# Kernel optimization log

Hardware: AMD Instinct MI355X
Metric: run time of the kernel (lower is better)

## Reference

```python
import jax, jax.numpy as jnp
import numpy as np


def setup_inputs() -> dict:
    key = jax.random.key(0)
    k1, k2 = jax.random.split(key)
    B, Ld, Lq, D = 32, 2048, 512, 256
    doc = jax.random.normal(k1, (B, Ld, D), dtype=jnp.float32)
    query = jax.random.normal(k2, (B, Lq, D), dtype=jnp.float32)
    doc_mask = jnp.ones((B, Ld), dtype=jnp.float32)
    q_mask = jnp.ones((B, Lq), dtype=jnp.float32)
    return {"doc": doc, "query": query, "doc_mask": doc_mask, "q_mask": q_mask}


def reference(doc, query, doc_mask, q_mask):
    # match_score: [B, Lq, Ld] = tanh(query @ doc^T)
    match_score = jnp.tanh(jnp.einsum('bqd,btd->bqt', query, doc))
    # sum over query positions -> [B, Ld]; softmax over doc positions
    query_to_doc_att = jax.nn.softmax(jnp.sum(match_score, axis=1), axis=-1)
    # sum over doc positions -> [B, Lq]; softmax over query positions
    doc_to_query_att = jax.nn.softmax(jnp.sum(match_score, axis=-1), axis=-1)
    # mask and renormalize
    alpha = query_to_doc_att * doc_mask
    alpha = alpha / jnp.sum(alpha, axis=1, keepdims=True)
    beta = doc_to_query_att * q_mask
    beta = beta / jnp.sum(beta, axis=1, keepdims=True)
    # weighted pooling: doc^T @ alpha -> [B, D]; query^T @ beta -> [B, D]
    doc_vector = jnp.einsum('btd,bt->bd', doc, alpha)
    que_vector = jnp.einsum('bqd,bq->bd', query, beta)
    return jnp.concatenate([doc_vector, que_vector], axis=1)  # [B, 2D]
```

## Files before the change

### kernel.cpp

```cpp
#include <hip/hip_runtime.h>
#include <hip/hip_bf16.h>
#include <cstdint>

#define BB 32
#define LD 2048
#define LQ 512
#define DD 256
#define BM 128
#define BN 128
#define BK 64

typedef _Float16 half8 __attribute__((ext_vector_type(8)));
typedef _Float16 half4 __attribute__((ext_vector_type(4)));
typedef float float4v __attribute__((ext_vector_type(4)));

__device__ __forceinline__ float tanh_fast(float x) {
    float e = __expf(2.0f * x);
    return 1.0f - 2.0f / (e + 1.0f);
}

__device__ __forceinline__ void load_lds16(const void* g, void* s) {
    __builtin_amdgcn_global_load_lds((const __attribute__((address_space(1))) void*)g,
                                     (__attribute__((address_space(3))) void*)s, 16, 0, 0);
}

#define DOCN8 (BB * LD * DD / 8)
#define QRYN8 (BB * LQ * DD / 8)

__global__ __launch_bounds__(256) void kconv(const float* __restrict__ doc,
                                             const float* __restrict__ qry,
                                             _Float16* __restrict__ dh,
                                             _Float16* __restrict__ qh) {
    int i = blockIdx.x * 256 + threadIdx.x;
    const float* src;
    _Float16* dst;
    int idx;
    if (i < DOCN8) { src = doc; dst = dh; idx = i; }
    else           { src = qry; dst = qh; idx = i - DOCN8; }
    const float4v* s = (const float4v*)src + (size_t)idx * 2;
    float4v a = s[0], c = s[1];
    half8 h = {(_Float16)a[0], (_Float16)a[1], (_Float16)a[2], (_Float16)a[3],
               (_Float16)c[0], (_Float16)c[1], (_Float16)c[2], (_Float16)c[3]};
    *((half8*)dst + idx) = h;
}

template <bool F16SRC>
__global__ __launch_bounds__(256) void k1(const void* __restrict__ qsrc,
                                          const void* __restrict__ dsrc,
                                          float* __restrict__ alog,
                                          float* __restrict__ blog) {
    __shared__ _Float16 sQ[BM * BK];
    __shared__ _Float16 sD[BN * BK];
    const int bq = blockIdx.x, bt = blockIdx.y, b = blockIdx.z;
    const int tid = threadIdx.x;
    const int lane = tid & 63;
    const int wave = tid >> 6;
    const int r16 = lane & 15;
    const int q4 = lane >> 4;
    const int mb = (wave >> 1) * 64, nb = (wave & 1) * 64;

    float4v acc[4][4];
    float4v zero = {0.f, 0.f, 0.f, 0.f};
#pragma unroll
    for (int m = 0; m < 4; m++)
#pragma unroll
        for (int n = 0; n < 4; n++) acc[m][n] = zero;

    const int lrow = lane >> 3;
    const int lcol = ((lane & 7) ^ lrow) * 8;

    for (int kk = 0; kk < DD; kk += BK) {
        __syncthreads();
        if constexpr (F16SRC) {
            const _Float16* Qh = (const _Float16*)qsrc + ((size_t)b * LQ + bq * BM) * DD;
            const _Float16* Dh = (const _Float16*)dsrc + ((size_t)b * LD + bt * BN) * DD;
#pragma unroll
            for (int j = 0; j < 4; j++) {
                int c = wave * 4 + j;
                int row = 8 * c + lrow;
                load_lds16(Qh + (size_t)row * DD + kk + lcol, &sQ[c * 512]);
                load_lds16(Dh + (size_t)row * DD + kk + lcol, &sD[c * 512]);
            }
        } else {
            const float* Qf = (const float*)qsrc + ((size_t)b * LQ + bq * BM) * DD;
            const float* Df = (const float*)dsrc + ((size_t)b * LD + bt * BN) * DD;
#pragma unroll
            for (int i = 0; i < 8; i++) {
                int f = tid + 256 * i;
                int row = f >> 4, c = f & 15;
                int c2 = c >> 1, hlf = c & 1;
                int p = c2 ^ (row & 7);
                float4v v = *(const float4v*)(Qf + (size_t)row * DD + kk + 4 * c);
                half4 h = {(_Float16)v[0], (_Float16)v[1], (_Float16)v[2], (_Float16)v[3]};
                *(half4*)(&sQ[row * BK + p * 8 + hlf * 4]) = h;
                float4v w = *(const float4v*)(Df + (size_t)row * DD + kk + 4 * c);
                half4 h2 = {(_Float16)w[0], (_Float16)w[1], (_Float16)w[2], (_Float16)w[3]};
                *(half4*)(&sD[row * BK + p * 8 + hlf * 4]) = h2;
            }
        }
        __syncthreads();

#pragma unroll
        for (int kk2 = 0; kk2 < 2; kk2++) {
            const int sw = ((4 * kk2 + q4) ^ (r16 & 7)) * 8;
            half8 af[4], bf[4];
#pragma unroll
            for (int m = 0; m < 4; m++) af[m] = *(const half8*)(&sQ[(mb + 16 * m + r16) * BK + sw]);
#pragma unroll
            for (int n = 0; n < 4; n++) bf[n] = *(const half8*)(&sD[(nb + 16 * n + r16) * BK + sw]);
#pragma unroll
            for (int m = 0; m < 4; m++)
#pragma unroll
                for (int n = 0; n < 4; n++)
                    acc[m][n] = __builtin_amdgcn_mfma_f32_16x16x32_f16(af[m], bf[n], acc[m][n], 0, 0, 0);
        }
    }

    float rsum[4][4];
    float csum[4];
#pragma unroll
    for (int m = 0; m < 4; m++)
#pragma unroll
        for (int r = 0; r < 4; r++) rsum[m][r] = 0.f;
#pragma unroll
    for (int n = 0; n < 4; n++) csum[n] = 0.f;

#pragma unroll
    for (int m = 0; m < 4; m++)
#pragma unroll
        for (int n = 0; n < 4; n++) {
            float t0 = tanh_fast(acc[m][n][0]);
            float t1 = tanh_fast(acc[m][n][1]);
            float t2 = tanh_fast(acc[m][n][2]);
            float t3 = tanh_fast(acc[m][n][3]);
            csum[n] += t0 + t1 + t2 + t3;
            rsum[m][0] += t0;
            rsum[m][1] += t1;
            rsum[m][2] += t2;
            rsum[m][3] += t3;
        }

#pragma unroll
    for (int m = 0; m < 4; m++) {
#pragma unroll
        for (int r = 0; r < 4; r++) {
            float v = rsum[m][r];
            v += __shfl_xor(v, 1);
            v += __shfl_xor(v, 2);
            v += __shfl_xor(v, 4);
            v += __shfl_xor(v, 8);
            rsum[m][r] = v;
        }
        if (r16 < 4) {
            float v = (r16 == 0) ? rsum[m][0] : (r16 == 1) ? rsum[m][1] : (r16 == 2) ? rsum[m][2] : rsum[m][3];
            atomicAdd(blog + b * LQ + bq * BM + mb + 16 * m + 4 * q4 + r16, v);
        }
    }
#pragma unroll
    for (int n = 0; n < 4; n++) {
        float v = csum[n];
        v += __shfl_xor(v, 16);
        v += __shfl_xor(v, 32);
        if (lane < 16) atomicAdd(alog + b * LD + bt * BN + nb + 16 * n + lane, v);
    }
}

__global__ __launch_bounds__(256) void k2(const float* __restrict__ alog, const float* __restrict__ blog,
                                          const float* __restrict__ dmask, const float* __restrict__ qmask,
                                          float* __restrict__ alpha, float* __restrict__ beta) {
    int blk = blockIdx.x;
    const float *lg, *mk;
    float* out;
    int n;
    if (blk < BB) {
        lg = alog + blk * LD; mk = dmask + blk * LD; out = alpha + blk * LD; n = LD;
    } else {
        int b = blk - BB;
        lg = blog + b * LQ; mk = qmask + b * LQ; out = beta + b * LQ; n = LQ;
    }
    int tid = threadIdx.x, lane = tid & 63, wave = tid >> 6;
    __shared__ float sm[4], ss[4];
    float mx = -3.0e38f;
    for (int i = tid; i < n; i += 256) mx = fmaxf(mx, lg[i]);
#pragma unroll
    for (int s = 1; s < 64; s <<= 1) mx = fmaxf(mx, __shfl_xor(mx, s));
    if (lane == 0) sm[wave] = mx;
    __syncthreads();
    mx = fmaxf(fmaxf(sm[0], sm[1]), fmaxf(sm[2], sm[3]));
    float sum = 0.f;
    for (int i = tid; i < n; i += 256) sum += __expf(lg[i] - mx) * mk[i];
#pragma unroll
    for (int s = 1; s < 64; s <<= 1) sum += __shfl_xor(sum, s);
    if (lane == 0) ss[wave] = sum;
    __syncthreads();
    sum = ss[0] + ss[1] + ss[2] + ss[3];
    float inv = 1.0f / sum;
    for (int i = tid; i < n; i += 256) out[i] = __expf(lg[i] - mx) * mk[i] * inv;
}

template <bool F16SRC>
__global__ __launch_bounds__(256) void k3(const float* __restrict__ docf, const float* __restrict__ qryf,
                                          const _Float16* __restrict__ dh, const _Float16* __restrict__ qh,
                                          const float* __restrict__ alpha, const float* __restrict__ beta,
                                          float* __restrict__ out) {
    __shared__ float sm[8 * DD];
    int blk = blockIdx.x, tid = threadIdx.x;
    const _Float16* srch;
    const float* srcf;
    const float* w;
    float* dst;
    if (blk < BB * 16) {
        int b = blk >> 4, ch = blk & 15;
        srch = dh + ((size_t)b * LD + ch * 128) * DD;
        srcf = docf + ((size_t)b * LD + ch * 128) * DD;
        w = alpha + b * LD + ch * 128;
        dst = out + b * 2 * DD;
    } else {
        int k = blk - BB * 16;
        int b = k >> 2, ch = k & 3;
        srch = qh + ((size_t)b * LQ + ch * 128) * DD;
        srcf = qryf + ((size_t)b * LQ + ch * 128) * DD;
        w = beta + b * LQ + ch * 128;
        dst = out + b * 2 * DD + DD;
    }
    int g = tid >> 5, c = tid & 31;
    float acc[8];
#pragma unroll
    for (int j = 0; j < 8; j++) acc[j] = 0.f;
    for (int r = 0; r < 16; r++) {
        int t = r * 8 + g;
        float wt = w[t];
        if constexpr (F16SRC) {
            half8 x = *(const half8*)(srch + (size_t)t * DD + c * 8);
#pragma unroll
            for (int j = 0; j < 8; j++) acc[j] += wt * (float)x[j];
        } else {
            const float4v* p = (const float4v*)(srcf + (size_t)t * DD + c * 8);
            float4v x0 = p[0], x1 = p[1];
#pragma unroll
            for (int j = 0; j < 4; j++) { acc[j] += wt * x0[j]; acc[4 + j] += wt * x1[j]; }
        }
    }
#pragma unroll
    for (int j = 0; j < 8; j++) sm[g * DD + c * 8 + j] = acc[j];
    __syncthreads();
    float s = 0.f;
#pragma unroll
    for (int g2 = 0; g2 < 8; g2++) s += sm[g2 * DD + tid];
    atomicAdd(dst + tid, s);
}

extern "C" void kernel_launch(void* const* d_in, const int* in_sizes, int n_in,
                              void* d_out, int out_size, void* d_ws, size_t ws_size,
                              hipStream_t stream) {
    (void)in_sizes; (void)n_in; (void)out_size;
    const float* doc = (const float*)d_in[0];
    const float* qry = (const float*)d_in[1];
    const float* dmask = (const float*)d_in[2];
    const float* qmask = (const float*)d_in[3];
    float* out = (float*)d_out;

    float* alog = (float*)d_ws;
    float* blog = alog + BB * LD;
    float* alpha = blog + BB * LQ;
    float* beta = alpha + BB * LD;
    _Float16* dh = (_Float16*)(beta + BB * LQ);
    _Float16* qh = dh + (size_t)BB * LD * DD;
    size_t needed = (size_t)(2 * BB * LD + 2 * BB * LQ) * 4 +
                    ((size_t)BB * LD * DD + (size_t)BB * LQ * DD) * 2;
    bool useF16 = ws_size >= needed;

    hipMemsetAsync(alog, 0, (size_t)(BB * LD + BB * LQ) * 4, stream);
    hipMemsetAsync(d_out, 0, (size_t)BB * 2 * DD * 4, stream);

    if (useF16) {
        kconv<<<(DOCN8 + QRYN8) / 256, 256, 0, stream>>>(doc, qry, dh, qh);
        k1<true><<<dim3(LQ / BM, LD / BN, BB), 256, 0, stream>>>(qh, dh, alog, blog);
    } else {
        k1<false><<<dim3(LQ / BM, LD / BN, BB), 256, 0, stream>>>(qry, doc, alog, blog);
    }
    k2<<<2 * BB, 256, 0, stream>>>(alog, blog, dmask, qmask, alpha, beta);
    if (useF16) {
        k3<true><<<BB * 16 + BB * 4, 256, 0, stream>>>(doc, qry, dh, qh, alpha, beta, out);
    } else {
        k3<false><<<BB * 16 + BB * 4, 256, 0, stream>>>(doc, qry, dh, qh, alpha, beta, out);
    }
}
```

Measured before the change: 169.1 us.

## Drop separate fp16 conversion pass and convert fp32 inputs inside GEMM loads

Removes the standalone kernel that converted doc and query to fp16 in workspace; the score GEMM now always loads fp32 from global memory and converts to fp16 while writing LDS, with precomputed per-thread addresses. The pooling kernel reads fp32 directly. This eliminates a full read/write pass over both inputs, at the cost of doubled global bytes in the GEMM loads and losing the async global-to-LDS path. Tanh and exp are also rewritten with exp2/rcp intrinsics.

```diff
diff --git a/kernel.cpp b/kernel.cpp
--- a/kernel.cpp
+++ b/kernel.cpp
@@ -15,38 +15,13 @@
 typedef float float4v __attribute__((ext_vector_type(4)));
 
 __device__ __forceinline__ float tanh_fast(float x) {
-    float e = __expf(2.0f * x);
-    return 1.0f - 2.0f / (e + 1.0f);
-}
-
-__device__ __forceinline__ void load_lds16(const void* g, void* s) {
-    __builtin_amdgcn_global_load_lds((const __attribute__((address_space(1))) void*)g,
-                                     (__attribute__((address_space(3))) void*)s, 16, 0, 0);
-}
-
-#define DOCN8 (BB * LD * DD / 8)
-#define QRYN8 (BB * LQ * DD / 8)
-
-__global__ __launch_bounds__(256) void kconv(const float* __restrict__ doc,
-                                             const float* __restrict__ qry,
-                                             _Float16* __restrict__ dh,
-                                             _Float16* __restrict__ qh) {
-    int i = blockIdx.x * 256 + threadIdx.x;
-    const float* src;
-    _Float16* dst;
-    int idx;
-    if (i < DOCN8) { src = doc; dst = dh; idx = i; }
-    else           { src = qry; dst = qh; idx = i - DOCN8; }
-    const float4v* s = (const float4v*)src + (size_t)idx * 2;
-    float4v a = s[0], c = s[1];
-    half8 h = {(_Float16)a[0], (_Float16)a[1], (_Float16)a[2], (_Float16)a[3],
-               (_Float16)c[0], (_Float16)c[1], (_Float16)c[2], (_Float16)c[3]};
-    *((half8*)dst + idx) = h;
-}
-
-template <bool F16SRC>
-__global__ __launch_bounds__(256) void k1(const void* __restrict__ qsrc,
-                                          const void* __restrict__ dsrc,
+    float t = __builtin_amdgcn_exp2f(x * 2.885390081777927f);
+    float r = __builtin_amdgcn_rcpf(t + 1.0f);
+    return fmaf(-2.0f, r, 1.0f);
+}
+
+__global__ __launch_bounds__(256) void k1(const float* __restrict__ qsrc,
+                                          const float* __restrict__ dsrc,
                                           float* __restrict__ alog,
                                           float* __restrict__ blog) {
     __shared__ _Float16 sQ[BM * BK];
@@ -66,37 +41,24 @@
 #pragma unroll
         for (int n = 0; n < 4; n++) acc[m][n] = zero;
 
-    const int lrow = lane >> 3;
-    const int lcol = ((lane & 7) ^ lrow) * 8;
+    const int r0 = tid >> 4;
+    const int c = tid & 15;
+    const int c2 = c >> 1, hlf = c & 1;
+    const int p = c2 ^ (r0 & 7);
+    const int ldsoff = r0 * BK + p * 8 + hlf * 4;
+    const float* Qf = qsrc + ((size_t)b * LQ + bq * BM) * DD + (size_t)r0 * DD + 4 * c;
+    const float* Df = dsrc + ((size_t)b * LD + bt * BN) * DD + (size_t)r0 * DD + 4 * c;
 
     for (int kk = 0; kk < DD; kk += BK) {
         __syncthreads();
-        if constexpr (F16SRC) {
-            const _Float16* Qh = (const _Float16*)qsrc + ((size_t)b * LQ + bq * BM) * DD;
-            const _Float16* Dh = (const _Float16*)dsrc + ((size_t)b * LD + bt * BN) * DD;
-#pragma unroll
-            for (int j = 0; j < 4; j++) {
-                int c = wave * 4 + j;
-                int row = 8 * c + lrow;
-                load_lds16(Qh + (size_t)row * DD + kk + lcol, &sQ[c * 512]);
-                load_lds16(Dh + (size_t)row * DD + kk + lcol, &sD[c * 512]);
-            }
-        } else {
-            const float* Qf = (const float*)qsrc + ((size_t)b * LQ + bq * BM) * DD;
-            const float* Df = (const float*)dsrc + ((size_t)b * LD + bt * BN) * DD;
-#pragma unroll
-            for (int i = 0; i < 8; i++) {
-                int f = tid + 256 * i;
-                int row = f >> 4, c = f & 15;
-                int c2 = c >> 1, hlf = c & 1;
-                int p = c2 ^ (row & 7);
-                float4v v = *(const float4v*)(Qf + (size_t)row * DD + kk + 4 * c);
-                half4 h = {(_Float16)v[0], (_Float16)v[1], (_Float16)v[2], (_Float16)v[3]};
-                *(half4*)(&sQ[row * BK + p * 8 + hlf * 4]) = h;
-                float4v w = *(const float4v*)(Df + (size_t)row * DD + kk + 4 * c);
-                half4 h2 = {(_Float16)w[0], (_Float16)w[1], (_Float16)w[2], (_Float16)w[3]};
-                *(half4*)(&sD[row * BK + p * 8 + hlf * 4]) = h2;
-            }
+#pragma unroll
+        for (int i = 0; i < 8; i++) {
+            float4v v = *(const float4v*)(Qf + kk + (size_t)i * 16 * DD);
+            half4 h = {(_Float16)v[0], (_Float16)v[1], (_Float16)v[2], (_Float16)v[3]};
+            *(half4*)(&sQ[ldsoff + i * 16 * BK]) = h;
+            float4v w = *(const float4v*)(Df + kk + (size_t)i * 16 * DD);
+            half4 h2 = {(_Float16)w[0], (_Float16)w[1], (_Float16)w[2], (_Float16)w[3]};
+            *(half4*)(&sD[ldsoff + i * 16 * BK]) = h2;
         }
         __syncthreads();
 
@@ -187,38 +149,35 @@
     if (lane == 0) sm[wave] = mx;
     __syncthreads();
     mx = fmaxf(fmaxf(sm[0], sm[1]), fmaxf(sm[2], sm[3]));
+    const float L2E = 1.4426950408889634f;
     float sum = 0.f;
-    for (int i = tid; i < n; i += 256) sum += __expf(lg[i] - mx) * mk[i];
+    for (int i = tid; i < n; i += 256) sum += __builtin_amdgcn_exp2f((lg[i] - mx) * L2E) * mk[i];
 #pragma unroll
     for (int s = 1; s < 64; s <<= 1) sum += __shfl_xor(sum, s);
     if (lane == 0) ss[wave] = sum;
     __syncthreads();
     sum = ss[0] + ss[1] + ss[2] + ss[3];
     float inv = 1.0f / sum;
-    for (int i = tid; i < n; i += 256) out[i] = __expf(lg[i] - mx) * mk[i] * inv;
-}
-
-template <bool F16SRC>
+    for (int i = tid; i < n; i += 256)
+        out[i] = __builtin_amdgcn_exp2f((lg[i] - mx) * L2E) * mk[i] * inv;
+}
+
 __global__ __launch_bounds__(256) void k3(const float* __restrict__ docf, const float* __restrict__ qryf,
-                                          const _Float16* __restrict__ dh, const _Float16* __restrict__ qh,
                                           const float* __restrict__ alpha, const float* __restrict__ beta,
                                           float* __restrict__ out) {
     __shared__ float sm[8 * DD];
     int blk = blockIdx.x, tid = threadIdx.x;
-    const _Float16* srch;
     const float* srcf;
     const float* w;
     float* dst;
     if (blk < BB * 16) {
         int b = blk >> 4, ch = blk & 15;
-        srch = dh + ((size_t)b * LD + ch * 128) * DD;
         srcf = docf + ((size_t)b * LD + ch * 128) * DD;
         w = alpha + b * LD + ch * 128;
         dst = out + b * 2 * DD;
     } else {
         int k = blk - BB * 16;
         int b = k >> 2, ch = k & 3;
-        srch = qh + ((size_t)b * LQ + ch * 128) * DD;
         srcf = qryf + ((size_t)b * LQ + ch * 128) * DD;
         w = beta + b * LQ + ch * 128;
         dst = out + b * 2 * DD + DD;
@@ -230,16 +189,10 @@
     for (int r = 0; r < 16; r++) {
         int t = r * 8 + g;
         float wt = w[t];
-        if constexpr (F16SRC) {
-            half8 x = *(const half8*)(srch + (size_t)t * DD + c * 8);
-#pragma unroll
-            for (int j = 0; j < 8; j++) acc[j] += wt * (float)x[j];
-        } else {
-            const float4v* p = (const float4v*)(srcf + (size_t)t * DD + c * 8);
-            float4v x0 = p[0], x1 = p[1];
-#pragma unroll
-            for (int j = 0; j < 4; j++) { acc[j] += wt * x0[j]; acc[4 + j] += wt * x1[j]; }
-        }
+        const float4v* p = (const float4v*)(srcf + (size_t)t * DD + c * 8);
+        float4v x0 = p[0], x1 = p[1];
+#pragma unroll
+        for (int j = 0; j < 4; j++) { acc[j] += wt * x0[j]; acc[4 + j] += wt * x1[j]; }
     }
 #pragma unroll
     for (int j = 0; j < 8; j++) sm[g * DD + c * 8 + j] = acc[j];
@@ -253,7 +206,7 @@
 extern "C" void kernel_launch(void* const* d_in, const int* in_sizes, int n_in,
                               void* d_out, int out_size, void* d_ws, size_t ws_size,
                               hipStream_t stream) {
-    (void)in_sizes; (void)n_in; (void)out_size;
+    (void)in_sizes; (void)n_in; (void)out_size; (void)ws_size;
     const float* doc = (const float*)d_in[0];
     const float* qry = (const float*)d_in[1];
     const float* dmask = (const float*)d_in[2];
@@ -264,25 +217,11 @@
     float* blog = alog + BB * LD;
     float* alpha = blog + BB * LQ;
     float* beta = alpha + BB * LD;
-    _Float16* dh = (_Float16*)(beta + BB * LQ);
-    _Float16* qh = dh + (size_t)BB * LD * DD;
-    size_t needed = (size_t)(2 * BB * LD + 2 * BB * LQ) * 4 +
-                    ((size_t)BB * LD * DD + (size_t)BB * LQ * DD) * 2;
-    bool useF16 = ws_size >= needed;
 
     hipMemsetAsync(alog, 0, (size_t)(BB * LD + BB * LQ) * 4, stream);
     hipMemsetAsync(d_out, 0, (size_t)BB * 2 * DD * 4, stream);
 
-    if (useF16) {
-        kconv<<<(DOCN8 + QRYN8) / 256, 256, 0, stream>>>(doc, qry, dh, qh);
-        k1<true><<<dim3(LQ / BM, LD / BN, BB), 256, 0, stream>>>(qh, dh, alog, blog);
-    } else {
-        k1<false><<<dim3(LQ / BM, LD / BN, BB), 256, 0, stream>>>(qry, doc, alog, blog);
-    }
+    k1<<<dim3(LQ / BM, LD / BN, BB), 256, 0, stream>>>(qry, doc, alog, blog);
     k2<<<2 * BB, 256, 0, stream>>>(alog, blog, dmask, qmask, alpha, beta);
-    if (useF16) {
-        k3<true><<<BB * 16 + BB * 4, 256, 0, stream>>>(doc, qry, dh, qh, alpha, beta, out);
-    } else {
-        k3<false><<<BB * 16 + BB * 4, 256, 0, stream>>>(doc, qry, dh, qh, alpha, beta, out);
-    }
-}
+    k3<<<BB * 16 + BB * 4, 256, 0, stream>>>(doc, qry, alpha, beta, out);
+}
```

Result: slower. 172.4 us (+2.0%).

## Replace global atomics with per-tile partial sums reduced in softmax kernel

Applied to the files above, without the earlier changes.

The GEMM-tanh kernel now reduces its row and column sums through shared memory and writes non-atomic per-tile partials into workspace slices, instead of issuing global atomicAdds. The softmax kernel then sums those partials, zeroes the output itself, and caches logits and exponentials in LDS so they are not recomputed. This removes both memsets and the atomic traffic, at the cost of a larger workspace and some extra partial-sum reads. Tanh and exp now use the hardware exp2 and reciprocal builtins, and the pooling loop is unrolled.

```diff
diff --git a/kernel.cpp b/kernel.cpp
--- a/kernel.cpp
+++ b/kernel.cpp
@@ -15,8 +15,9 @@
 typedef float float4v __attribute__((ext_vector_type(4)));
 
 __device__ __forceinline__ float tanh_fast(float x) {
-    float e = __expf(2.0f * x);
-    return 1.0f - 2.0f / (e + 1.0f);
+    float t = __builtin_amdgcn_exp2f(x * 2.885390081777927f);
+    float r = __builtin_amdgcn_rcpf(t + 1.0f);
+    return fmaf(-2.0f, r, 1.0f);
 }
 
 __device__ __forceinline__ void load_lds16(const void* g, void* s) {
@@ -47,10 +48,12 @@
 template <bool F16SRC>
 __global__ __launch_bounds__(256) void k1(const void* __restrict__ qsrc,
                                           const void* __restrict__ dsrc,
-                                          float* __restrict__ alog,
-                                          float* __restrict__ blog) {
+                                          float* __restrict__ pa,
+                                          float* __restrict__ pb) {
     __shared__ _Float16 sQ[BM * BK];
     __shared__ _Float16 sD[BN * BK];
+    __shared__ float srow[BM][2];
+    __shared__ float scol[BN][2];
     const int bq = blockIdx.x, bt = blockIdx.y, b = blockIdx.z;
     const int tid = threadIdx.x;
     const int lane = tid & 63;
@@ -153,7 +156,7 @@
         }
         if (r16 < 4) {
             float v = (r16 == 0) ? rsum[m][0] : (r16 == 1) ? rsum[m][1] : (r16 == 2) ? rsum[m][2] : rsum[m][3];
-            atomicAdd(blog + b * LQ + bq * BM + mb + 16 * m + 4 * q4 + r16, v);
+            srow[mb + 16 * m + 4 * q4 + r16][wave & 1] = v;
         }
     }
 #pragma unroll
@@ -161,41 +164,74 @@
         float v = csum[n];
         v += __shfl_xor(v, 16);
         v += __shfl_xor(v, 32);
-        if (lane < 16) atomicAdd(alog + b * LD + bt * BN + nb + 16 * n + lane, v);
-    }
-}
-
-__global__ __launch_bounds__(256) void k2(const float* __restrict__ alog, const float* __restrict__ blog,
+        if (lane < 16) scol[nb + 16 * n + lane][wave >> 1] = v;
+    }
+    __syncthreads();
+    if (tid < 128) {
+        float v = srow[tid][0] + srow[tid][1];
+        pb[((size_t)bt * BB + b) * LQ + bq * BM + tid] = v;
+        float u = scol[tid][0] + scol[tid][1];
+        pa[((size_t)bq * BB + b) * LD + bt * BN + tid] = u;
+    }
+}
+
+__global__ __launch_bounds__(256) void k2(const float* __restrict__ pa, const float* __restrict__ pb,
                                           const float* __restrict__ dmask, const float* __restrict__ qmask,
-                                          float* __restrict__ alpha, float* __restrict__ beta) {
-    int blk = blockIdx.x;
-    const float *lg, *mk;
-    float* out;
+                                          float* __restrict__ alpha, float* __restrict__ beta,
+                                          float* __restrict__ out) {
+    __shared__ float sl[2048];
+    __shared__ float sm[4], ss[4];
+    int blk = blockIdx.x, tid = threadIdx.x, lane = tid & 63, wave = tid >> 6;
+    const float* mk;
+    float* dst;
     int n;
     if (blk < BB) {
-        lg = alog + blk * LD; mk = dmask + blk * LD; out = alpha + blk * LD; n = LD;
+        int b = blk;
+        out[b * 2 * DD + tid] = 0.f;
+        out[b * 2 * DD + 256 + tid] = 0.f;
+        n = LD;
+        mk = dmask + b * LD;
+        dst = alpha + b * LD;
+        for (int i = tid; i < n; i += 256) {
+            float s = 0.f;
+#pragma unroll
+            for (int j = 0; j < 4; j++) s += pa[((size_t)j * BB + b) * LD + i];
+            sl[i] = s;
+        }
     } else {
         int b = blk - BB;
-        lg = blog + b * LQ; mk = qmask + b * LQ; out = beta + b * LQ; n = LQ;
-    }
-    int tid = threadIdx.x, lane = tid & 63, wave = tid >> 6;
-    __shared__ float sm[4], ss[4];
+        n = LQ;
+        mk = qmask + b * LQ;
+        dst = beta + b * LQ;
+        for (int i = tid; i < n; i += 256) {
+            float s = 0.f;
+#pragma unroll
+            for (int j = 0; j < 16; j++) s += pb[((size_t)j * BB + b) * LQ + i];
+            sl[i] = s;
+        }
+    }
+    __syncthreads();
     float mx = -3.0e38f;
-    for (int i = tid; i < n; i += 256) mx = fmaxf(mx, lg[i]);
+    for (int i = tid; i < n; i += 256) mx = fmaxf(mx, sl[i]);
 #pragma unroll
     for (int s = 1; s < 64; s <<= 1) mx = fmaxf(mx, __shfl_xor(mx, s));
     if (lane == 0) sm[wave] = mx;
     __syncthreads();
     mx = fmaxf(fmaxf(sm[0], sm[1]), fmaxf(sm[2], sm[3]));
+    const float L2E = 1.4426950408889634f;
     float sum = 0.f;
-    for (int i = tid; i < n; i += 256) sum += __expf(lg[i] - mx) * mk[i];
+    for (int i = tid; i < n; i += 256) {
+        float e = __builtin_amdgcn_exp2f((sl[i] - mx) * L2E) * mk[i];
+        sl[i] = e;
+        sum += e;
+    }
 #pragma unroll
     for (int s = 1; s < 64; s <<= 1) sum += __shfl_xor(sum, s);
     if (lane == 0) ss[wave] = sum;
     __syncthreads();
     sum = ss[0] + ss[1] + ss[2] + ss[3];
     float inv = 1.0f / sum;
-    for (int i = tid; i < n; i += 256) out[i] = __expf(lg[i] - mx) * mk[i] * inv;
+    for (int i = tid; i < n; i += 256) dst[i] = sl[i] * inv;
 }
 
 template <bool F16SRC>
@@ -205,21 +241,21 @@
                                           float* __restrict__ out) {
     __shared__ float sm[8 * DD];
     int blk = blockIdx.x, tid = threadIdx.x;
+    const float* srcf;
     const _Float16* srch;
-    const float* srcf;
     const float* w;
     float* dst;
     if (blk < BB * 16) {
         int b = blk >> 4, ch = blk & 15;
+        srcf = docf + ((size_t)b * LD + ch * 128) * DD;
         srch = dh + ((size_t)b * LD + ch * 128) * DD;
-        srcf = docf + ((size_t)b * LD + ch * 128) * DD;
         w = alpha + b * LD + ch * 128;
         dst = out + b * 2 * DD;
     } else {
         int k = blk - BB * 16;
         int b = k >> 2, ch = k & 3;
+        srcf = qryf + ((size_t)b * LQ + ch * 128) * DD;
         srch = qh + ((size_t)b * LQ + ch * 128) * DD;
-        srcf = qryf + ((size_t)b * LQ + ch * 128) * DD;
         w = beta + b * LQ + ch * 128;
         dst = out + b * 2 * DD + DD;
     }
@@ -227,6 +263,7 @@
     float acc[8];
 #pragma unroll
     for (int j = 0; j < 8; j++) acc[j] = 0.f;
+#pragma unroll
     for (int r = 0; r < 16; r++) {
         int t = r * 8 + g;
         float wt = w[t];
@@ -260,26 +297,23 @@
     const float* qmask = (const float*)d_in[3];
     float* out = (float*)d_out;
 
-    float* alog = (float*)d_ws;
-    float* blog = alog + BB * LD;
-    float* alpha = blog + BB * LQ;
+    float* pa = (float*)d_ws;
+    float* pb = pa + 4 * BB * LD;
+    float* alpha = pb + 16 * BB * LQ;
     float* beta = alpha + BB * LD;
     _Float16* dh = (_Float16*)(beta + BB * LQ);
     _Float16* qh = dh + (size_t)BB * LD * DD;
-    size_t needed = (size_t)(2 * BB * LD + 2 * BB * LQ) * 4 +
+    size_t needed = (size_t)(4 * BB * LD + 16 * BB * LQ + BB * LD + BB * LQ) * 4 +
                     ((size_t)BB * LD * DD + (size_t)BB * LQ * DD) * 2;
     bool useF16 = ws_size >= needed;
 
-    hipMemsetAsync(alog, 0, (size_t)(BB * LD + BB * LQ) * 4, stream);
-    hipMemsetAsync(d_out, 0, (size_t)BB * 2 * DD * 4, stream);
-
     if (useF16) {
         kconv<<<(DOCN8 + QRYN8) / 256, 256, 0, stream>>>(doc, qry, dh, qh);
-        k1<true><<<dim3(LQ / BM, LD / BN, BB), 256, 0, stream>>>(qh, dh, alog, blog);
+        k1<true><<<dim3(LQ / BM, LD / BN, BB), 256, 0, stream>>>(qh, dh, pa, pb);
     } else {
-        k1<false><<<dim3(LQ / BM, LD / BN, BB), 256, 0, stream>>>(qry, doc, alog, blog);
-    }
-    k2<<<2 * BB, 256, 0, stream>>>(alog, blog, dmask, qmask, alpha, beta);
+        k1<false><<<dim3(LQ / BM, LD / BN, BB), 256, 0, stream>>>(qry, doc, pa, pb);
+    }
+    k2<<<2 * BB, 256, 0, stream>>>(pa, pb, dmask, qmask, alpha, beta, out);
     if (useF16) {
         k3<true><<<BB * 16 + BB * 4, 256, 0, stream>>>(doc, qry, dh, qh, alpha, beta, out);
     } else {
```

New measurement: 159.8 us. 1.06x faster.
